# Kernel tuning notes

Hardware: AMD Instinct MI355X
Metric: run time of the kernel (lower is better)

Reference implementation:

```python
import jax, jax.numpy as jnp
import numpy as np

C_CLIP = 10.0  # Bello et al. logit clipping constant (init arg C)


def setup_inputs() -> dict:
    key = jax.random.key(0)
    k1, k2, k3, k4, k5 = jax.random.split(key, 5)
    B, S, D = 64, 2048, 512
    scale = 1.0 / np.sqrt(D)  # ~torch Linear default init scale
    src = jax.random.normal(k1, (B, S, D), dtype=jnp.float32)
    tgt = jax.random.normal(k2, (B, 1, D), dtype=jnp.float32)
    W_q = jax.random.normal(k3, (D, D), dtype=jnp.float32) * scale
    W_ref = jax.random.normal(k4, (D, D), dtype=jnp.float32) * scale
    v = jax.random.uniform(k5, (D,), dtype=jnp.float32)  # uniform_(0, 1) as in source
    return {"src": src, "tgt": tgt, "W_q": W_q, "W_ref": W_ref, "v": v}


def reference(src, tgt, W_q, W_ref, v):
    # h = tanh(W_q(tgt) + W_ref(src))  -> [B, S, D] (tgt broadcasts over S)
    h = jnp.tanh(tgt @ W_q.T + src @ W_ref.T)
    # u = bmm(v, h^T) -> [B, 1, S]
    u = jnp.einsum("bsd,d->bs", h, v)[:, None, :]
    # logit clipping: C * tanh(u)
    logit = C_CLIP * jnp.tanh(u)
    probs = jax.nn.softmax(logit, axis=-1)  # [B, 1, S]
    # d_prime = bmm(probs, src) -> [B, 1, D]  ('Sup' path glimpse)
    d_prime = jnp.einsum("bqs,bsd->bqd", probs, src)
    return (d_prime, probs, logit)
```

## Files before the change

kernel.cpp:

```cpp
#include <hip/hip_runtime.h>
#include <math.h>

#define NB 64
#define NS 2048
#define ND 512
#define MTOT (NB * NS)
#define CCLIP 10.0f

typedef _Float16 f16x8 __attribute__((ext_vector_type(8)));
typedef _Float16 f16x4 __attribute__((ext_vector_type(4)));
typedef float f32x4 __attribute__((ext_vector_type(4)));

__device__ __forceinline__ float tanh_fast(float x) {
  float e = __expf(2.f * x);
  return 1.f - 2.f * __builtin_amdgcn_rcpf(e + 1.f);
}

__global__ __launch_bounds__(256) void cvtw2_kernel(
    const float* __restrict__ Wref, _Float16* __restrict__ Wc) {
  const int g = blockIdx.x * 256 + threadIdx.x;
  const int lane = g & 63;
  const int rest = g >> 6;
  const int c32 = rest & 31;
  const int kt = rest >> 5;
  const int col = c32 * 16 + (lane & 15);
  const int k = kt * 32 + ((lane >> 4) & 3) * 8;
  const float4* in = (const float4*)(Wref + (size_t)col * ND + k);
  float4 a = in[0];
  float4 b = in[1];
  f16x8 o;
  o[0] = (_Float16)a.x; o[1] = (_Float16)a.y;
  o[2] = (_Float16)a.z; o[3] = (_Float16)a.w;
  o[4] = (_Float16)b.x; o[5] = (_Float16)b.y;
  o[6] = (_Float16)b.z; o[7] = (_Float16)b.w;
  *(f16x8*)(Wc + (size_t)g * 8) = o;
}

__global__ __launch_bounds__(256) void qk_kernel(const float* __restrict__ tgt,
                                                 const float* __restrict__ Wq,
                                                 float* __restrict__ q_ws) {
  const int b = blockIdx.x >> 1;
  const int d = ((blockIdx.x & 1) << 8) + threadIdx.x;
  __shared__ float tl[ND];
  tl[threadIdx.x] = tgt[b * ND + threadIdx.x];
  tl[threadIdx.x + 256] = tgt[b * ND + threadIdx.x + 256];
  __syncthreads();
  const float4* wr = (const float4*)(Wq + (size_t)d * ND);
  float acc = 0.f;
#pragma unroll 8
  for (int k4 = 0; k4 < ND / 4; ++k4) {
    float4 w4 = wr[k4];
    acc += w4.x * tl[4 * k4 + 0] + w4.y * tl[4 * k4 + 1] +
           w4.z * tl[4 * k4 + 2] + w4.w * tl[4 * k4 + 3];
  }
  q_ws[b * ND + d] = acc;
}

__global__ __launch_bounds__(256, 2) void gemm_kernel(
    const float* __restrict__ src, const _Float16* __restrict__ Wc,
    const float* __restrict__ q_ws, const float* __restrict__ v,
    float* __restrict__ out_logit, float* __restrict__ out_probs_w,
    float* __restrict__ dp_ws) {
  __shared__ __align__(16) _Float16 sAall[2 * 4 * 64 * 8];
  __shared__ float ured[4 * 64];
  __shared__ float wsh[64];

  const int tid = threadIdx.x;
  const int lane = tid & 63;
  const int w = tid >> 6;
  const int cq = w;
  const int s0 = blockIdx.x << 6;
  const int bb = blockIdx.x >> 5;

  const int quad = lane >> 4;
  const int l15 = lane & 15;

  const int ar = tid >> 2;
  const int akg = tid & 3;
  const float4* ap =
      (const float4*)(src + ((size_t)(s0 + ar) << 9)) + akg * 2;
  const int aoff = akg * 512 + ((ar ^ (akg << 2)) << 3);

  const _Float16* wb = Wc + ((size_t)(cq * 8) * 64 + lane) * 8;

  f32x4 acc[4][8];
#pragma unroll
  for (int i = 0; i < 4; ++i)
#pragma unroll
    for (int j = 0; j < 8; ++j) acc[i][j] = (f32x4){0.f, 0.f, 0.f, 0.f};

  {
    float4 x0 = ap[0];
    float4 x1 = ap[1];
    f16x8 hh;
    hh[0] = (_Float16)x0.x; hh[1] = (_Float16)x0.y;
    hh[2] = (_Float16)x0.z; hh[3] = (_Float16)x0.w;
    hh[4] = (_Float16)x1.x; hh[5] = (_Float16)x1.y;
    hh[6] = (_Float16)x1.z; hh[7] = (_Float16)x1.w;
    *(f16x8*)(sAall + aoff) = hh;
  }
  __syncthreads();

  for (int kt = 0; kt < 16; ++kt) {
    const _Float16* sA = sAall + (kt & 1) * 2048;

    f16x8 bf[8];
    const _Float16* wk = wb + (size_t)(kt * 32) * 512;
#pragma unroll
    for (int j = 0; j < 8; ++j)
      bf[j] = *(const f16x8*)(wk + (size_t)j * 512);

    f16x8 af[4];
#pragma unroll
    for (int i = 0; i < 4; ++i) {
      const int row = 16 * i + l15;
      af[i] = *(const f16x8*)(sA + quad * 512 + ((row ^ (quad << 2)) << 3));
    }

    if (kt < 15) {
      float4 x0 = ap[(kt + 1) * 8];
      float4 x1 = ap[(kt + 1) * 8 + 1];
      f16x8 hh;
      hh[0] = (_Float16)x0.x; hh[1] = (_Float16)x0.y;
      hh[2] = (_Float16)x0.z; hh[3] = (_Float16)x0.w;
      hh[4] = (_Float16)x1.x; hh[5] = (_Float16)x1.y;
      hh[6] = (_Float16)x1.z; hh[7] = (_Float16)x1.w;
      *(f16x8*)(sAall + ((kt + 1) & 1) * 2048 + aoff) = hh;
    }

#pragma unroll
    for (int i = 0; i < 4; ++i)
#pragma unroll
      for (int j = 0; j < 8; ++j)
        acc[i][j] = __builtin_amdgcn_mfma_f32_16x16x32_f16(af[i], bf[j],
                                                           acc[i][j], 0, 0, 0);

    __syncthreads();
  }

  float pu[4][4];
#pragma unroll
  for (int i = 0; i < 4; ++i)
#pragma unroll
    for (int r = 0; r < 4; ++r) pu[i][r] = 0.f;

#pragma unroll
  for (int j = 0; j < 8; ++j) {
    const int dl = cq * 128 + 16 * j + l15;
    const float qq = q_ws[bb * ND + dl];
    const float vv = v[dl];
#pragma unroll
    for (int i = 0; i < 4; ++i) {
      f32x4 a = acc[i][j];
#pragma unroll
      for (int r = 0; r < 4; ++r) pu[i][r] += tanh_fast(a[r] + qq) * vv;
    }
  }

#pragma unroll
  for (int i = 0; i < 4; ++i)
#pragma unroll
    for (int r = 0; r < 4; ++r) {
      float x = pu[i][r];
      x += __shfl_xor(x, 1, 16);
      x += __shfl_xor(x, 2, 16);
      x += __shfl_xor(x, 4, 16);
      x += __shfl_xor(x, 8, 16);
      pu[i][r] = x;
    }

  if (l15 == 0) {
#pragma unroll
    for (int i = 0; i < 4; ++i)
#pragma unroll
      for (int r = 0; r < 4; ++r)
        ured[w * 64 + 16 * i + quad * 4 + r] = pu[i][r];
  }
  __syncthreads();
  if (tid < 64) {
    const float u =
        ured[tid] + ured[64 + tid] + ured[128 + tid] + ured[192 + tid];
    const float lg = CCLIP * tanhf(u);
    out_logit[s0 + tid] = lg;
    const float wexp = expf(lg - CCLIP);
    out_probs_w[s0 + tid] = wexp;
    wsh[tid] = wexp;
  }
  __syncthreads();

  const int c4 = tid & 127;
  const int half = tid >> 7;
  const float4* sp = (const float4*)(src + ((size_t)s0 << 9)) + c4;
  float dx = 0.f, dy = 0.f, dz = 0.f, dw = 0.f;
  const int r0 = half << 5;
#pragma unroll 4
  for (int r = r0; r < r0 + 32; ++r) {
    const float wr = wsh[r];
    const float4 x = sp[(size_t)r * 128];
    dx += wr * x.x; dy += wr * x.y; dz += wr * x.z; dw += wr * x.w;
  }
  float4* red4 = (float4*)sAall;
  if (half) {
    float4 o; o.x = dx; o.y = dy; o.z = dz; o.w = dw;
    red4[c4] = o;
  }
  __syncthreads();
  if (!half) {
    float4 o = red4[c4];
    o.x += dx; o.y += dy; o.z += dz; o.w += dw;
    *(float4*)(dp_ws + (size_t)blockIdx.x * ND + (c4 << 2)) = o;
  }
}

__global__ __launch_bounds__(256) void fin_kernel(
    const float* __restrict__ dp_ws, float* __restrict__ out_dp,
    float* __restrict__ out_probs) {
  const int b = blockIdx.x;
  const int tid = threadIdx.x;
  __shared__ float red[4];
  __shared__ float s_inv;

  float x = 0.f;
  for (int idx = tid; idx < NS; idx += 256) x += out_probs[b * NS + idx];
#pragma unroll
  for (int m = 32; m; m >>= 1) x += __shfl_xor(x, m, 64);
  if ((tid & 63) == 0) red[tid >> 6] = x;
  __syncthreads();
  if (tid == 0) s_inv = 1.f / (red[0] + red[1] + red[2] + red[3]);
  __syncthreads();
  const float inv = s_inv;

  for (int idx = tid; idx < NS; idx += 256)
    out_probs[b * NS + idx] *= inv;

  for (int d = tid; d < ND; d += 256) {
    float acc = 0.f;
#pragma unroll 8
    for (int ch = 0; ch < 32; ++ch)
      acc += dp_ws[(size_t)(b * 32 + ch) * ND + d];
    out_dp[b * ND + d] = acc * inv;
  }
}

extern "C" void kernel_launch(void* const* d_in, const int* in_sizes, int n_in,
                              void* d_out, int out_size, void* d_ws,
                              size_t ws_size, hipStream_t stream) {
  const float* src = (const float*)d_in[0];
  const float* tgt = (const float*)d_in[1];
  const float* Wq = (const float*)d_in[2];
  const float* Wref = (const float*)d_in[3];
  const float* v = (const float*)d_in[4];

  float* out = (float*)d_out;
  float* out_dp = out;
  float* out_probs = out + NB * ND;
  float* out_logit = out + NB * ND + NB * NS;

  char* ws = (char*)d_ws;
  _Float16* Wc = (_Float16*)ws;
  float* q_ws = (float*)(ws + 524288);
  float* dp_ws = (float*)(ws + 655360);

  cvtw2_kernel<<<128, 256, 0, stream>>>(Wref, Wc);
  qk_kernel<<<2 * NB, 256, 0, stream>>>(tgt, Wq, q_ws);
  gemm_kernel<<<MTOT / 64, 256, 0, stream>>>(src, Wc, q_ws, v, out_logit,
                                             out_probs, dp_ws);
  fin_kernel<<<NB, 256, 0, stream>>>(dp_ws, out_dp, out_probs);
}
```

Before: 453.9 us.

## Stage full 64x512 fp16 src tile in LDS before GEMM, drop per-k syncs

The GEMM kernel now loads and converts the block's entire 64-row src tile (64x512 fp16, 64 KB) into a swizzled LDS buffer up front. This replaces the two-stage double buffer that fetched one 32-wide k slice per iteration. The MFMA loop then reads only from LDS and no longer needs a barrier each k step. The aim is more memory-level parallelism for the src loads and less synchronisation. In exchange, loads no longer overlap MFMA inside a block, and LDS use per block rises sharply, which may limit how many blocks fit per CU.

```diff
diff --git a/kernel.cpp b/kernel.cpp
--- a/kernel.cpp
+++ b/kernel.cpp
@@ -61,7 +61,7 @@
     const float* __restrict__ q_ws, const float* __restrict__ v,
     float* __restrict__ out_logit, float* __restrict__ out_probs_w,
     float* __restrict__ dp_ws) {
-  __shared__ __align__(16) _Float16 sAall[2 * 4 * 64 * 8];
+  __shared__ __align__(16) _Float16 sA[64 * 512];
   __shared__ float ured[4 * 64];
   __shared__ float wsh[64];
 
@@ -75,35 +75,33 @@
   const int quad = lane >> 4;
   const int l15 = lane & 15;
 
-  const int ar = tid >> 2;
-  const int akg = tid & 3;
-  const float4* ap =
-      (const float4*)(src + ((size_t)(s0 + ar) << 9)) + akg * 2;
-  const int aoff = akg * 512 + ((ar ^ (akg << 2)) << 3);
-
-  const _Float16* wb = Wc + ((size_t)(cq * 8) * 64 + lane) * 8;
-
-  f32x4 acc[4][8];
-#pragma unroll
-  for (int i = 0; i < 4; ++i)
-#pragma unroll
-    for (int j = 0; j < 8; ++j) acc[i][j] = (f32x4){0.f, 0.f, 0.f, 0.f};
-
-  {
-    float4 x0 = ap[0];
-    float4 x1 = ap[1];
+#pragma unroll 4
+  for (int it = 0; it < 16; ++it) {
+    const int c = it * 256 + tid;
+    const int row = c >> 6;
+    const int k8 = c & 63;
+    const float4* g =
+        (const float4*)(src + (((size_t)(s0 + row)) << 9) + k8 * 8);
+    float4 x0 = g[0];
+    float4 x1 = g[1];
     f16x8 hh;
     hh[0] = (_Float16)x0.x; hh[1] = (_Float16)x0.y;
     hh[2] = (_Float16)x0.z; hh[3] = (_Float16)x0.w;
     hh[4] = (_Float16)x1.x; hh[5] = (_Float16)x1.y;
     hh[6] = (_Float16)x1.z; hh[7] = (_Float16)x1.w;
-    *(f16x8*)(sAall + aoff) = hh;
-  }
-  __syncthreads();
+    *(f16x8*)(sA + k8 * 512 + ((row ^ (k8 & 7)) << 3)) = hh;
+  }
+  __syncthreads();
+
+  const _Float16* wb = Wc + ((size_t)(cq * 8) * 64 + lane) * 8;
+
+  f32x4 acc[4][8];
+#pragma unroll
+  for (int i = 0; i < 4; ++i)
+#pragma unroll
+    for (int j = 0; j < 8; ++j) acc[i][j] = (f32x4){0.f, 0.f, 0.f, 0.f};
 
   for (int kt = 0; kt < 16; ++kt) {
-    const _Float16* sA = sAall + (kt & 1) * 2048;
-
     f16x8 bf[8];
     const _Float16* wk = wb + (size_t)(kt * 32) * 512;
 #pragma unroll
@@ -111,21 +109,11 @@
       bf[j] = *(const f16x8*)(wk + (size_t)j * 512);
 
     f16x8 af[4];
+    const int k8r = kt * 4 + quad;
 #pragma unroll
     for (int i = 0; i < 4; ++i) {
       const int row = 16 * i + l15;
-      af[i] = *(const f16x8*)(sA + quad * 512 + ((row ^ (quad << 2)) << 3));
-    }
-
-    if (kt < 15) {
-      float4 x0 = ap[(kt + 1) * 8];
-      float4 x1 = ap[(kt + 1) * 8 + 1];
-      f16x8 hh;
-      hh[0] = (_Float16)x0.x; hh[1] = (_Float16)x0.y;
-      hh[2] = (_Float16)x0.z; hh[3] = (_Float16)x0.w;
-      hh[4] = (_Float16)x1.x; hh[5] = (_Float16)x1.y;
-      hh[6] = (_Float16)x1.z; hh[7] = (_Float16)x1.w;
-      *(f16x8*)(sAall + ((kt + 1) & 1) * 2048 + aoff) = hh;
+      af[i] = *(const f16x8*)(sA + k8r * 512 + ((row ^ (k8r & 7)) << 3));
     }
 
 #pragma unroll
@@ -134,8 +122,6 @@
       for (int j = 0; j < 8; ++j)
         acc[i][j] = __builtin_amdgcn_mfma_f32_16x16x32_f16(af[i], bf[j],
                                                            acc[i][j], 0, 0, 0);
-
-    __syncthreads();
   }
 
   float pu[4][4];
@@ -199,7 +185,7 @@
     const float4 x = sp[(size_t)r * 128];
     dx += wr * x.x; dy += wr * x.y; dz += wr * x.z; dw += wr * x.w;
   }
-  float4* red4 = (float4*)sAall;
+  float4* red4 = (float4*)sA;
   if (half) {
     float4 o; o.x = dx; o.y = dy; o.z = dz; o.w = dw;
     red4[c4] = o;
```

After: 471.1 us. 3.8% more time.
